# Optimization experiments

Measured on AMD Instinct MI355X. Metric: run time of the kernel, lower is better.

Reference implementation:

```python
import jax, jax.numpy as jnp
import numpy as np
from jax import lax

B, T, S = 32, 64, 400
H, E, EMB, V = 512, 1024, 256, 32000


def setup_inputs() -> dict:
    key = jax.random.key(0)
    ks = jax.random.split(key, 16)
    w = lambda k, shape: jax.random.normal(k, shape, dtype=jnp.float32) * 0.05
    return {
        "target": jax.random.randint(ks[0], (B, T), 0, V),
        "h0": jax.random.normal(ks[1], (B, H), dtype=jnp.float32),
        "c0": jax.random.normal(ks[2], (B, H), dtype=jnp.float32),
        "enc_outs": jax.random.normal(ks[3], (S, B, E), dtype=jnp.float32),
        "attn_mask": jnp.ones((B, S), dtype=jnp.int32),
        "emb": w(ks[4], (V, EMB)),
        "W_ih": w(ks[5], (4 * H, EMB)),
        "b_ih": w(ks[6], (4 * H,)),
        "W_hh": w(ks[7], (4 * H, H)),
        "b_hh": w(ks[8], (4 * H,)),
        "W_attn": w(ks[9], (H, E)),
        "b_attn": w(ks[10], (H,)),
        "W_concat": w(ks[11], (H, E + H)),
        "b_concat": w(ks[12], (H,)),
        "W_out": w(ks[13], (V, H)),
        "b_out": w(ks[14], (V,)),
    }


def reference(target, h0, c0, enc_outs, attn_mask, emb, W_ih, b_ih, W_hh, b_hh,
              W_attn, b_attn, W_concat, b_concat, W_out, b_out):
    # Precompute attention keys projection once: [S, B, H]
    keys_proj = jnp.einsum("sbe,he->sbh", enc_outs, W_attn) + b_attn
    masked = attn_mask == 0  # [B, S]
    x_seq = emb[target].transpose(1, 0, 2)  # [T, B, EMB]

    def step(carry, x_t):
        h, c = carry
        # LSTMCell (torch gate order: i, f, g, o)
        gates = x_t @ W_ih.T + b_ih + h @ W_hh.T + b_hh  # [B, 4H]
        i, f, g, o = jnp.split(gates, 4, axis=1)
        c = jax.nn.sigmoid(f) * c + jax.nn.sigmoid(i) * jnp.tanh(g)
        h = jax.nn.sigmoid(o) * jnp.tanh(c)
        # additive-style attention: sum over hidden of query*key_proj
        scores = jnp.einsum("bh,sbh->bs", h, keys_proj)  # [B, S]
        scores = jnp.where(masked, jnp.float32(-1e18), scores)
        a = jax.nn.softmax(scores, axis=1)
        ctx = jnp.einsum("bs,sbe->be", a, enc_outs)  # [B, E]
        cat = jnp.tanh(jnp.concatenate([ctx, h], axis=1) @ W_concat.T + b_concat)
        logit = jax.nn.log_softmax(cat @ W_out.T + b_out, axis=-1)  # [B, V]
        return (h, c), logit

    (_, _), logits = lax.scan(step, (h0, c0), x_seq)  # [T, B, V]
    return logits.transpose(1, 0, 2)  # [B, T, V]
```

## Files before the change

kernel.cpp:

```cpp
#include <hip/hip_runtime.h>
#include <hip/hip_bf16.h>
#include <hip/hip_fp16.h>

#define B_ 32
#define T_ 64
#define S_ 400
#define SPAD_ 512
#define H_ 512
#define E_ 1024
#define EMB_ 256
#define V_ 32000
#define NCB_ 500

#define KEYS_BLOCKS 200
#define CVT_BLOCKS 48
#define MEGA_BLOCKS (8 + KEYS_BLOCKS + CVT_BLOCKS)
#define MEGA_LDS (65536 + 33280 + 4096 + 32)

typedef _Float16 f16;
typedef _Float16 half8 __attribute__((ext_vector_type(8)));
typedef float f32x4 __attribute__((ext_vector_type(4)));
typedef float f32x16 __attribute__((ext_vector_type(16)));
typedef unsigned uint4v __attribute__((ext_vector_type(4)));

__device__ __forceinline__ void gl_lds16(const void* g, void* l) {
  __builtin_amdgcn_global_load_lds(
      (const __attribute__((address_space(1))) void*)g,
      (__attribute__((address_space(3))) void*)l, 16, 0, 0);
}

__device__ __forceinline__ float sigmoidf_(float x) { return 1.f / (1.f + expf(-x)); }

__device__ __forceinline__ uint4v load_b128_sys(const void* p) {
  uint4v r;
  asm volatile("global_load_dwordx4 %0, %1, off sc0 sc1" : "=v"(r) : "v"(p) : "memory");
  return r;
}
__device__ __forceinline__ void store_b128_sys(void* p, uint4v v) {
  asm volatile("global_store_dwordx4 %0, %1, off sc0 sc1" :: "v"(p), "v"(v) : "memory");
}

__global__ __launch_bounds__(256) void prep_kernel(const float* __restrict__ b_ih,
                                                   const float* __restrict__ b_hh,
                                                   float* __restrict__ biasperm,
                                                   const float* __restrict__ Whh,
                                                   f16* __restrict__ Wperm,
                                                   const float* __restrict__ Wih,
                                                   f16* __restrict__ Wihp,
                                                   const float* __restrict__ h0,
                                                   f16* __restrict__ hbuf,
                                                   const float* __restrict__ Wattn,
                                                   f16* __restrict__ Wattn_f,
                                                   const int* __restrict__ target,
                                                   const float* __restrict__ emb,
                                                   f16* __restrict__ xin) {
  int idx = blockIdx.x * 256 + threadIdx.x;
  if (idx < 4 * H_) {
    int j = idx >> 2, gg = idx & 3;
    biasperm[idx] = b_ih[gg * H_ + j] + b_hh[gg * H_ + j];
  }
  if (idx < B_ * H_) hbuf[idx] = (f16)h0[idx];
  if (idx < T_ * B_ * H_ / 8) {
    uint4v p = {0xFFFFFFFFu, 0xFFFFFFFFu, 0xFFFFFFFFu, 0xFFFFFFFFu};
    reinterpret_cast<uint4v*>(reinterpret_cast<char*>(hbuf) + (size_t)B_ * H_ * 2)[idx] = p;
  }
  {
    int j = idx >> 9, k = idx & 511;
#pragma unroll
    for (int gg = 0; gg < 4; ++gg)
      Wperm[((size_t)(j * 4 + gg)) * H_ + k] = (f16)Whh[((size_t)(gg * H_ + j)) * H_ + k];
  }
  if (idx < H_ * EMB_) {
    int j = idx >> 8, k = idx & 255;
#pragma unroll
    for (int gg = 0; gg < 4; ++gg)
      Wihp[((size_t)(j * 4 + gg)) * EMB_ + k] = (f16)Wih[((size_t)(gg * H_ + j)) * EMB_ + k];
  }
  {
    float2 v = reinterpret_cast<const float2*>(Wattn)[idx];
    union { f16 h[2]; unsigned u; } o;
    o.h[0] = (f16)v.x; o.h[1] = (f16)v.y;
    reinterpret_cast<unsigned*>(Wattn_f)[idx] = o.u;
  }
  {
    int rr = idx >> 7, cc = (idx & 127) * 2;
    int t = rr >> 5, bb = rr & 31;
    int tok = target[bb * T_ + t];
    float2 ev = *reinterpret_cast<const float2*>(emb + (size_t)tok * EMB_ + cc);
    union { f16 h[2]; unsigned u; } o2;
    o2.h[0] = (f16)ev.x; o2.h[1] = (f16)ev.y;
    *reinterpret_cast<unsigned*>(xin + (size_t)rr * EMB_ + cc) = o2.u;
  }
}

template <int OUTK, bool DO_TANH>
__global__ __launch_bounds__(256) void gemm_bt_kernel(const f16* __restrict__ A,
                                                      const f16* __restrict__ W,
                                                      const float* __restrict__ bias,
                                                      void* __restrict__ outp,
                                                      int M, int N, int K) {
  __shared__ __align__(16) char As[128 * 64];
  __shared__ __align__(16) char Bs[128 * 64];
  const int tid = threadIdx.x;
  const int lane = tid & 63, wave = tid >> 6;
  const int wr = (wave >> 1) * 64, wc = (wave & 1) * 64;
  const int fr = lane & 15, fq = lane >> 4;
  const int row0 = blockIdx.x * 128, col0 = blockIdx.y * 128;

  f32x4 acc[4][4];
#pragma unroll
  for (int i = 0; i < 4; ++i)
#pragma unroll
    for (int j = 0; j < 4; ++j) acc[i][j] = {0.f, 0.f, 0.f, 0.f};

  for (int k0 = 0; k0 < K; k0 += 32) {
    __syncthreads();
#pragma unroll
    for (int i = 0; i < 2; ++i) {
      int o = tid * 16 + i * 4096;
      int r = o >> 6, kk = (o & 63) >> 1;
      gl_lds16(A + (size_t)(row0 + r) * K + (k0 + kk), As + o);
      gl_lds16(W + (size_t)(col0 + r) * K + (k0 + kk), Bs + o);
    }
    __syncthreads();
    half8 af[4], bfr[4];
#pragma unroll
    for (int mi = 0; mi < 4; ++mi)
      af[mi] = *reinterpret_cast<const half8*>(As + (wr + mi * 16 + fr) * 64 + fq * 16);
#pragma unroll
    for (int ni = 0; ni < 4; ++ni)
      bfr[ni] = *reinterpret_cast<const half8*>(Bs + (wc + ni * 16 + fr) * 64 + fq * 16);
#pragma unroll
    for (int mi = 0; mi < 4; ++mi)
#pragma unroll
      for (int ni = 0; ni < 4; ++ni)
        acc[mi][ni] = __builtin_amdgcn_mfma_f32_16x16x32_f16(af[mi], bfr[ni], acc[mi][ni], 0, 0, 0);
  }

#pragma unroll
  for (int mi = 0; mi < 4; ++mi)
#pragma unroll
    for (int ni = 0; ni < 4; ++ni)
#pragma unroll
      for (int r = 0; r < 4; ++r) {
        int row = row0 + wr + mi * 16 + fq * 4 + r;
        int col = col0 + wc + ni * 16 + fr;
        float v = acc[mi][ni][r] + bias[col];
        if (DO_TANH) v = tanhf(v);
        if (OUTK == 0) {
          ((float*)outp)[(size_t)row * N + col] = v;
        } else if (OUTK == 1) {
          ((f16*)outp)[(size_t)row * N + col] = (f16)v;
        } else {
          int orow = (row & 31) * T_ + (row >> 5);
          ((float*)outp)[(size_t)orow * N + col] = v;
        }
      }
}

__global__ __launch_bounds__(512, 1) void mega_kernel(
    const float* __restrict__ xpart, const f16* __restrict__ Wperm,
    const float* __restrict__ c0, f16* __restrict__ hbuf,
    const float* __restrict__ enc, const f16* __restrict__ Wattn_f,
    const float* __restrict__ b_attn, f16* __restrict__ keys,
    const float* __restrict__ wc_src, f16* __restrict__ wc_dst,
    const float* __restrict__ wo_src, f16* __restrict__ wo_dst) {
  extern __shared__ char lds[];
  const int blk = blockIdx.x, tid = threadIdx.x;
  const int lane = tid & 63, wave = tid >> 6;

  if (blk < 8) {
    char* Abuf = lds;
    float* gates = (float*)(lds + 65536);
    unsigned* hstage = (unsigned*)(lds + 65536 + 33280);
    int* flags = (int*)(lds + 65536 + 33280 + 4096);
    const int g = blk;
    const int ln31 = lane & 31, lh = lane >> 5;

    if (tid < 8) flags[tid] = 0;

    half8 wf[32];
    {
      const f16* wrow = Wperm + ((size_t)(g * 256 + wave * 32 + ln31)) * H_ + lh * 8;
#pragma unroll
      for (int kc = 0; kc < 32; ++kc)
        wf[kc] = *reinterpret_cast<const half8*>(wrow + kc * 16);
    }

    const int b = tid >> 4, qd = tid & 15;
    float cst[4];
#pragma unroll
    for (int jj = 0; jj < 4; ++jj)
      cst[jj] = c0[b * H_ + g * 64 + qd * 4 + jj];

    __syncthreads();

    for (int t = 0; t < T_; ++t) {
      const float* xr = xpart + ((size_t)(t * B_ + b)) * (4 * H_) + g * 256 + qd * 16;
      float4 xv[4];
#pragma unroll
      for (int i = 0; i < 4; ++i) xv[i] = *reinterpret_cast<const float4*>(xr + i * 4);

      {
        int p = (t == 0) ? wave : (wave + (wave >= g ? 1 : 0));
        bool duty = (t == 0) ? true : (wave < 7);
        if (duty) {
          const char* sb = (const char*)hbuf + (size_t)t * 32768 + ln31 * 1024 + p * 128 + lh * 16;
          while (true) {
            uint4v v0 = load_b128_sys(sb);
            uint4v v1 = load_b128_sys(sb + 32);
            uint4v v2 = load_b128_sys(sb + 64);
            uint4v v3 = load_b128_sys(sb + 96);
            asm volatile("s_waitcnt vmcnt(0)" ::: "memory");
            __builtin_amdgcn_sched_barrier(0);
            unsigned bad = 0;
#pragma unroll
            for (int d = 0; d < 4; ++d)
              bad |= (unsigned)(v0[d] == 0xFFFFFFFFu) | (unsigned)(v1[d] == 0xFFFFFFFFu) |
                     (unsigned)(v2[d] == 0xFFFFFFFFu) | (unsigned)(v3[d] == 0xFFFFFFFFu);
            if (__all(bad == 0)) {
              char* ab = Abuf + (size_t)(t & 1) * 32768 + lane * 16;
              *(uint4v*)(ab + (size_t)(4 * p + 0) * 1024) = v0;
              *(uint4v*)(ab + (size_t)(4 * p + 1) * 1024) = v1;
              *(uint4v*)(ab + (size_t)(4 * p + 2) * 1024) = v2;
              *(uint4v*)(ab + (size_t)(4 * p + 3) * 1024) = v3;
              asm volatile("s_waitcnt lgkmcnt(0)" ::: "memory");
              __builtin_amdgcn_sched_barrier(0);
              if (lane == 0)
                __hip_atomic_fetch_add(&flags[p], 1, __ATOMIC_RELAXED,
                                       __HIP_MEMORY_SCOPE_WORKGROUP);
              break;
            }
          }
        }
      }

      f32x16 acc;
#pragma unroll
      for (int r = 0; r < 16; ++r) acc[r] = 0.f;
      const char* abR = Abuf + (size_t)(t & 1) * 32768 + lane * 16;
      const char* hsR = (const char*)hstage + lane * 16;
      const int thr = t + 1;
#pragma unroll
      for (int ps = 0; ps < 8; ++ps) {
        if (ps == g && t > 0) {
#pragma unroll
          for (int c = 0; c < 4; ++c) {
            half8 a = *(const half8*)(hsR + c * 1024);
            acc = __builtin_amdgcn_mfma_f32_32x32x16_f16(a, wf[4 * ps + c], acc, 0, 0, 0);
          }
        } else {
          while (__hip_atomic_load(&flags[ps], __ATOMIC_ACQUIRE,
                                   __HIP_MEMORY_SCOPE_WORKGROUP) < thr) {}
#pragma unroll
          for (int c = 0; c < 4; ++c) {
            half8 a = *(const half8*)(abR + (size_t)(4 * ps + c) * 1024);
            acc = __builtin_amdgcn_mfma_f32_32x32x16_f16(a, wf[4 * ps + c], acc, 0, 0, 0);
          }
        }
      }
#pragma unroll
      for (int r = 0; r < 16; ++r) {
        int row = (r & 3) + 8 * (r >> 2) + 4 * lh;
        gates[row * 260 + wave * 32 + ln31] = acc[r];
      }
      __syncthreads();

      const float* gr = &gates[b * 260 + qd * 16];
      float hv[4];
#pragma unroll
      for (int jj = 0; jj < 4; ++jj) {
        float gi = gr[jj * 4 + 0] + xv[jj].x;
        float gf = gr[jj * 4 + 1] + xv[jj].y;
        float gg = gr[jj * 4 + 2] + xv[jj].z;
        float go = gr[jj * 4 + 3] + xv[jj].w;
        cst[jj] = sigmoidf_(gf) * cst[jj] + sigmoidf_(gi) * tanhf(gg);
        hv[jj] = sigmoidf_(go) * tanhf(cst[jj]);
      }
      union { f16 h[2]; unsigned u; } pk0, pk1;
      pk0.h[0] = (f16)hv[0]; pk0.h[1] = (f16)hv[1];
      pk1.h[0] = (f16)hv[2]; pk1.h[1] = (f16)hv[3];
      {
        int cp0 = 2 * qd, cp1 = 2 * qd + 1;
        hstage[((cp0 >> 3) * 64 + ((cp0 >> 2) & 1) * 32 + b) * 4 + (cp0 & 3)] = pk0.u;
        hstage[((cp1 >> 3) * 64 + ((cp1 >> 2) & 1) * 32 + b) * 4 + (cp1 & 3)] = pk1.u;
      }
      __syncthreads();

      if (tid < 256) {
        int kcl = tid >> 6, l2 = tid & 63;
        uint4v v = *(const uint4v*)((const char*)hstage + (kcl * 64 + l2) * 16);
        store_b128_sys((char*)hbuf + (size_t)(t + 1) * 32768 + (l2 & 31) * 1024 +
                           g * 128 + kcl * 32 + (l2 >> 5) * 16,
                       v);
      }
    }
  } else if (blk < 8 + KEYS_BLOCKS) {
    char* As = lds;
    char* Bs = lds + 16384;
    const int kid = blk - 8;
    const int row0 = (kid % 50) * 256, col0 = (kid / 50) * 128;
    const int wr = (wave >> 1) * 64, wc = (wave & 1) * 64;
    const int fr = lane & 15, fq = lane >> 4;

    f32x4 acc[4][4];
#pragma unroll
    for (int i = 0; i < 4; ++i)
#pragma unroll
      for (int j = 0; j < 4; ++j) acc[i][j] = {0.f, 0.f, 0.f, 0.f};

    for (int k0 = 0; k0 < E_; k0 += 32) {
      __syncthreads();
      float4 av[4];
#pragma unroll
      for (int i = 0; i < 4; ++i) {
        int idx = tid + i * 512;
        int r = idx >> 3, ck = (idx & 7) * 4;
        av[i] = *reinterpret_cast<const float4*>(enc + (size_t)(row0 + r) * E_ + k0 + ck);
      }
      {
        int o = tid * 16;
        int r = o >> 6, kk = (o & 63) >> 1;
        gl_lds16(Wattn_f + (size_t)(col0 + r) * E_ + (k0 + kk), Bs + o);
      }
#pragma unroll
      for (int i = 0; i < 4; ++i) {
        int idx = tid + i * 512;
        int r = idx >> 3, ck = (idx & 7) * 4;
        union { f16 h[4]; unsigned long long u; } p;
        p.h[0] = (f16)av[i].x; p.h[1] = (f16)av[i].y;
        p.h[2] = (f16)av[i].z; p.h[3] = (f16)av[i].w;
        *reinterpret_cast<unsigned long long*>(As + r * 64 + ck * 2) = p.u;
      }
      __syncthreads();
      half8 af[4], bf[4];
#pragma unroll
      for (int mi = 0; mi < 4; ++mi)
        af[mi] = *reinterpret_cast<const half8*>(As + (wr + mi * 16 + fr) * 64 + fq * 16);
#pragma unroll
      for (int ni = 0; ni < 4; ++ni)
        bf[ni] = *reinterpret_cast<const half8*>(Bs + (wc + ni * 16 + fr) * 64 + fq * 16);
#pragma unroll
      for (int mi = 0; mi < 4; ++mi)
#pragma unroll
        for (int ni = 0; ni < 4; ++ni)
          acc[mi][ni] = __builtin_amdgcn_mfma_f32_16x16x32_f16(af[mi], bf[ni], acc[mi][ni], 0, 0, 0);
    }
#pragma unroll
    for (int mi = 0; mi < 4; ++mi)
#pragma unroll
      for (int ni = 0; ni < 4; ++ni)
#pragma unroll
        for (int r = 0; r < 4; ++r) {
          int row = row0 + wr + mi * 16 + fq * 4 + r;
          int col = col0 + wc + ni * 16 + fr;
          keys[(size_t)row * H_ + col] = (f16)(acc[mi][ni][r] + b_attn[col]);
        }
  } else {
    const int N2WC = H_ * (E_ + H_) / 2, N2WO = V_ * H_ / 2;
    const int total = N2WC + N2WO;
    const int stride = CVT_BLOCKS * 512;
    for (int i = (blk - 8 - KEYS_BLOCKS) * 512 + tid; i < total; i += stride) {
      const float* s; f16* d; int j;
      if (i < N2WC) { s = wc_src; d = wc_dst; j = i; }
      else { s = wo_src; d = wo_dst; j = i - N2WC; }
      float2 v = reinterpret_cast<const float2*>(s)[j];
      union { f16 h[2]; unsigned u; } o;
      o.h[0] = (f16)v.x; o.h[1] = (f16)v.y;
      reinterpret_cast<unsigned*>(d)[j] = o.u;
    }
  }
}

__global__ __launch_bounds__(256) void scores_mfma_kernel(const f16* __restrict__ keys,
                                                          const f16* __restrict__ hseq,
                                                          float* __restrict__ attnw) {
  const int b = blockIdx.y;
  const int lane = threadIdx.x & 63, wave = threadIdx.x >> 6;
  const int ln31 = lane & 31, lh = lane >> 5;
  const int stile = blockIdx.x * 128 + wave * 32;
  const f16* ar  = keys + ((size_t)(stile + ln31) * B_ + b) * H_ + lh * 8;
  const f16* br0 = hseq + ((size_t)ln31 * B_ + b) * H_ + lh * 8;
  const f16* br1 = hseq + ((size_t)(ln31 + 32) * B_ + b) * H_ + lh * 8;
  f32x16 ac0, ac1;
#pragma unroll
  for (int r = 0; r < 16; ++r) { ac0[r] = 0.f; ac1[r] = 0.f; }
#pragma unroll
  for (int kc = 0; kc < 32; ++kc) {
    half8 a  = *reinterpret_cast<const half8*>(ar + kc * 16);
    half8 h0 = *reinterpret_cast<const half8*>(br0 + kc * 16);
    half8 h1 = *reinterpret_cast<const half8*>(br1 + kc * 16);
    ac0 = __builtin_amdgcn_mfma_f32_32x32x16_f16(a, h0, ac0, 0, 0, 0);
    ac1 = __builtin_amdgcn_mfma_f32_32x32x16_f16(a, h1, ac1, 0, 0, 0);
  }
#pragma unroll
  for (int r = 0; r < 16; ++r) {
    int s = stile + (r & 3) + 8 * (r >> 2) + 4 * lh;
    if (s < S_) {
      attnw[((size_t)b * S_ + s) * T_ + ln31]      = ac0[r];
      attnw[((size_t)b * S_ + s) * T_ + 32 + ln31] = ac1[r];
    }
  }
}

__global__ __launch_bounds__(64) void softmax_kernel(float* __restrict__ attnw,
                                                     const int* __restrict__ mask) {
  int b = blockIdx.x, t = blockIdx.y, l = threadIdx.x;
  float vals[7];
  float m = -3.4e38f;
#pragma unroll
  for (int i = 0; i < 7; ++i) {
    int s = l + i * 64;
    float v = -3.4e38f;
    if (s < S_) {
      v = attnw[((size_t)b * S_ + s) * T_ + t];
      if (mask[b * S_ + s] == 0) v = -1e18f;
    }
    vals[i] = v;
    m = fmaxf(m, v);
  }
#pragma unroll
  for (int o = 32; o > 0; o >>= 1) m = fmaxf(m, __shfl_xor(m, o));
  float sum = 0.f;
#pragma unroll
  for (int i = 0; i < 7; ++i) {
    int s = l + i * 64;
    if (s < S_) { float e = expf(vals[i] - m); vals[i] = e; sum += e; }
  }
#pragma unroll
  for (int o = 32; o > 0; o >>= 1) sum += __shfl_xor(sum, o);
  float inv = 1.f / sum;
#pragma unroll
  for (int i = 0; i < 7; ++i) {
    int s = l + i * 64;
    if (s < S_) attnw[((size_t)b * S_ + s) * T_ + t] = vals[i] * inv;
  }
}

__global__ __launch_bounds__(256) void ctx_cat_kernel(const float* __restrict__ attnw,
                                                      const float* __restrict__ enc,
                                                      const f16* __restrict__ hseq,
                                                      f16* __restrict__ catin) {
  int b = blockIdx.x, y = blockIdx.y;
  if (y == 16) {
    for (int i = threadIdx.x; i < 64 * 64; i += 256) {
      int t = i >> 6, c = i & 63;
      uint4v v = *(const uint4v*)((const char*)hseq + ((size_t)t * B_ + b) * 1024 + c * 16);
      *(uint4v*)((char*)catin + ((size_t)t * B_ + b) * 3072 + 2048 + c * 16) = v;
    }
    return;
  }
  int e0 = y * 64;
  int el = threadIdx.x & 63, tq = threadIdx.x >> 6;
  __shared__ float a_lds[100 * 64];
  float acc[16];
#pragma unroll
  for (int i = 0; i < 16; ++i) acc[i] = 0.f;
  for (int scn = 0; scn < 4; ++scn) {
    __syncthreads();
    for (int i = threadIdx.x; i < 6400; i += 256)
      a_lds[i] = attnw[((size_t)b * S_ + scn * 100) * T_ + i];
    __syncthreads();
    for (int sl = 0; sl < 100; ++sl) {
      int s = scn * 100 + sl;
      float v = enc[((size_t)s * B_ + b) * E_ + e0 + el];
#pragma unroll
      for (int i = 0; i < 16; ++i) acc[i] += a_lds[sl * 64 + tq * 16 + i] * v;
    }
  }
#pragma unroll
  for (int i = 0; i < 16; ++i) {
    int t = tq * 16 + i;
    catin[((size_t)t * B_ + b) * (E_ + H_) + e0 + el] = (f16)acc[i];
  }
}

__global__ __launch_bounds__(512) void gemm_out256_kernel(const f16* __restrict__ A,
                                                          const f16* __restrict__ W,
                                                          const float* __restrict__ bias,
                                                          f16* __restrict__ lbuf,
                                                          float* __restrict__ pm,
                                                          float* __restrict__ ps) {
  __shared__ __align__(16) char As[256 * 64];
  __shared__ __align__(16) char Bs[128 * 64];
  const int tid = threadIdx.x;
  const int lane = tid & 63, wave = tid >> 6;
  const int wr = (wave >> 1) * 64, wc = (wave & 1) * 64;
  const int fr = lane & 15, fq = lane >> 4;
  const int row0 = blockIdx.x * 256, col0 = blockIdx.y * 128;

  f32x4 acc[4][4];
#pragma unroll
  for (int i = 0; i < 4; ++i)
#pragma unroll
    for (int j = 0; j < 4; ++j) acc[i][j] = {0.f, 0.f, 0.f, 0.f};

  for (int k0 = 0; k0 < H_; k0 += 32) {
    __syncthreads();
    {
      int o = tid * 16;
      int r = o >> 6, kk = (o & 63) >> 1;
      gl_lds16(A + (size_t)(row0 + r) * H_ + (k0 + kk), As + o);
      gl_lds16(W + (size_t)(col0 + r) * H_ + (k0 + kk), Bs + o);
      o += 8192; r = o >> 6; kk = (o & 63) >> 1;
      gl_lds16(A + (size_t)(row0 + r) * H_ + (k0 + kk), As + o);
    }
    __syncthreads();
    half8 af[4], bfr[4];
#pragma unroll
    for (int mi = 0; mi < 4; ++mi)
      af[mi] = *reinterpret_cast<const half8*>(As + (wr + mi * 16 + fr) * 64 + fq * 16);
#pragma unroll
    for (int ni = 0; ni < 4; ++ni)
      bfr[ni] = *reinterpret_cast<const half8*>(Bs + (wc + ni * 16 + fr) * 64 + fq * 16);
#pragma unroll
    for (int mi = 0; mi < 4; ++mi)
#pragma unroll
      for (int ni = 0; ni < 4; ++ni)
        acc[mi][ni] = __builtin_amdgcn_mfma_f32_16x16x32_f16(af[mi], bfr[ni], acc[mi][ni], 0, 0, 0);
  }

#pragma unroll
  for (int mi = 0; mi < 4; ++mi)
#pragma unroll
    for (int r = 0; r < 4; ++r) {
      int row = row0 + wr + mi * 16 + fq * 4 + r;
      float v0 = acc[mi][0][r] + bias[col0 + wc + fr];
      float v1 = acc[mi][1][r] + bias[col0 + wc + 16 + fr];
      float v2 = acc[mi][2][r] + bias[col0 + wc + 32 + fr];
      float v3 = acc[mi][3][r] + bias[col0 + wc + 48 + fr];
      f16* lp = lbuf + (size_t)row * V_ + col0 + wc + fr;
      lp[0] = (f16)v0; lp[16] = (f16)v1; lp[32] = (f16)v2; lp[48] = (f16)v3;
      float mx = fmaxf(fmaxf(v0, v1), fmaxf(v2, v3));
#pragma unroll
      for (int d2 = 1; d2 <= 8; d2 <<= 1) mx = fmaxf(mx, __shfl_xor(mx, d2));
      float sm = expf(v0 - mx) + expf(v1 - mx) + expf(v2 - mx) + expf(v3 - mx);
#pragma unroll
      for (int d2 = 1; d2 <= 8; d2 <<= 1) sm += __shfl_xor(sm, d2);
      if (fr == 0) {
        int cb = (col0 + wc) >> 6;
        pm[(size_t)row * NCB_ + cb] = mx;
        ps[(size_t)row * NCB_ + cb] = sm;
      }
    }
}

__global__ __launch_bounds__(256) void final_out_kernel(const f16* __restrict__ lbuf,
                                                        const float* __restrict__ pm,
                                                        const float* __restrict__ ps,
                                                        float* __restrict__ out) {
  int j = blockIdx.x;
  int b = j >> 6, t = j & 63;
  int r = t * B_ + b;
  int tid = threadIdx.x;
  __shared__ float red[4];
  __shared__ float lsh;

  float mv0 = -3.4e38f, sv0 = 0.f, mv1 = -3.4e38f, sv1 = 0.f;
  if (tid < NCB_) { mv0 = pm[(size_t)r * NCB_ + tid]; sv0 = ps[(size_t)r * NCB_ + tid]; }
  int i2 = tid + 256;
  if (i2 < NCB_) { mv1 = pm[(size_t)r * NCB_ + i2]; sv1 = ps[(size_t)r * NCB_ + i2]; }
  float m = fmaxf(mv0, mv1);
#pragma unroll
  for (int o = 32; o > 0; o >>= 1) m = fmaxf(m, __shfl_xor(m, o));
  if ((tid & 63) == 0) red[tid >> 6] = m;
  __syncthreads();
  float mm = fmaxf(fmaxf(red[0], red[1]), fmaxf(red[2], red[3]));
  float s = sv0 * expf(mv0 - mm) + sv1 * expf(mv1 - mm);
#pragma unroll
  for (int o = 32; o > 0; o >>= 1) s += __shfl_xor(s, o);
  __syncthreads();
  if ((tid & 63) == 0) red[tid >> 6] = s;
  __syncthreads();
  if (tid == 0) lsh = mm + logf(red[0] + red[1] + red[2] + red[3]);
  __syncthreads();
  float l = lsh;

  const half8* src = reinterpret_cast<const half8*>(lbuf + (size_t)r * V_);
  float4* dst = reinterpret_cast<float4*>(out + (size_t)j * V_);
  for (int c = tid; c < V_ / 8; c += 256) {
    half8 h = src[c];
    float4 o1, o2;
    o1.x = (float)h[0] - l; o1.y = (float)h[1] - l;
    o1.z = (float)h[2] - l; o1.w = (float)h[3] - l;
    o2.x = (float)h[4] - l; o2.y = (float)h[5] - l;
    o2.z = (float)h[6] - l; o2.w = (float)h[7] - l;
    dst[c * 2] = o1; dst[c * 2 + 1] = o2;
  }
}

__global__ __launch_bounds__(512, 1) void logsm_kernel(float* __restrict__ out) {
  int r = blockIdx.x;
  size_t base = (size_t)r * V_;
  int tid = threadIdx.x;
  float4* op = reinterpret_cast<float4*>(out + base);
  float4 v[16];
  float m = -3.4e38f;
#pragma unroll
  for (int k = 0; k < 16; ++k) {
    int c = tid + (k << 9);
    if (c < 8000) {
      v[k] = op[c];
      m = fmaxf(m, fmaxf(fmaxf(v[k].x, v[k].y), fmaxf(v[k].z, v[k].w)));
    }
  }
  __shared__ float red[8];
#pragma unroll
  for (int o = 32; o > 0; o >>= 1) m = fmaxf(m, __shfl_xor(m, o));
  if ((tid & 63) == 0) red[tid >> 6] = m;
  __syncthreads();
  float mm = red[0];
#pragma unroll
  for (int i = 1; i < 8; ++i) mm = fmaxf(mm, red[i]);
  float s = 0.f;
#pragma unroll
  for (int k = 0; k < 16; ++k) {
    int c = tid + (k << 9);
    if (c < 8000)
      s += expf(v[k].x - mm) + expf(v[k].y - mm) + expf(v[k].z - mm) + expf(v[k].w - mm);
  }
#pragma unroll
  for (int o = 32; o > 0; o >>= 1) s += __shfl_xor(s, o);
  __syncthreads();
  if ((tid & 63) == 0) red[tid >> 6] = s;
  __syncthreads();
  s = 0.f;
#pragma unroll
  for (int i = 0; i < 8; ++i) s += red[i];
  float lse = mm + logf(s);
#pragma unroll
  for (int k = 0; k < 16; ++k) {
    int c = tid + (k << 9);
    if (c < 8000) {
      float4 o4;
      o4.x = v[k].x - lse; o4.y = v[k].y - lse;
      o4.z = v[k].z - lse; o4.w = v[k].w - lse;
      op[c] = o4;
    }
  }
}

extern "C" void kernel_launch(void* const* d_in, const int* in_sizes, int n_in,
                              void* d_out, int out_size, void* d_ws, size_t ws_size,
                              hipStream_t stream) {
  const int*   target = (const int*)d_in[0];
  const float* h0     = (const float*)d_in[1];
  const float* c0     = (const float*)d_in[2];
  const float* enc    = (const float*)d_in[3];
  const int*   mask   = (const int*)d_in[4];
  const float* emb    = (const float*)d_in[5];
  const float* W_ih   = (const float*)d_in[6];
  const float* b_ih   = (const float*)d_in[7];
  const float* W_hh   = (const float*)d_in[8];
  const float* b_hh   = (const float*)d_in[9];
  const float* W_attn = (const float*)d_in[10];
  const float* b_attn = (const float*)d_in[11];
  const float* W_cat  = (const float*)d_in[12];
  const float* b_cat  = (const float*)d_in[13];
  const float* W_out  = (const float*)d_in[14];
  const float* b_out  = (const float*)d_in[15];

  char* ws = (char*)d_ws;
  size_t off = 0;
  auto alloc = [&](size_t bytes) {
    void* p = ws + off;
    off = (off + bytes + 255) & ~(size_t)255;
    return p;
  };
  f16*   keys_f   = (f16*)alloc((size_t)SPAD_ * B_ * H_ * 2);
  f16*   Wattn_f  = (f16*)alloc((size_t)H_ * E_ * 2);
  f16*   Wcat_f   = (f16*)alloc((size_t)H_ * (E_ + H_) * 2);
  f16*   Wout_f   = (f16*)alloc((size_t)V_ * H_ * 2);
  f16*   Wperm    = (f16*)alloc((size_t)4 * H_ * H_ * 2);
  f16*   Wihp     = (f16*)alloc((size_t)4 * H_ * EMB_ * 2);
  float* biasperm = (float*)alloc((size_t)4 * H_ * 4);
  f16*   xin_f    = (f16*)alloc((size_t)T_ * B_ * EMB_ * 2);
  float* xpart    = (float*)alloc((size_t)T_ * B_ * 4 * H_ * 4);
  f16*   catin_f  = (f16*)alloc((size_t)T_ * B_ * (E_ + H_) * 2);
  float* attnw    = (float*)alloc((size_t)B_ * S_ * T_ * 4);
  f16*   catbuf_f = (f16*)alloc((size_t)T_ * B_ * H_ * 2);
  f16*   hbuf     = (f16*)alloc((size_t)(T_ + 1) * B_ * H_ * 2);

  size_t extra = ((size_t)T_ * B_ * V_ * 2 + 255 + (size_t)T_ * B_ * NCB_ * 4 * 2 + 512);
  bool pathA = (off + extra) <= ws_size;
  f16* lbuf = nullptr; float* pm = nullptr; float* psb = nullptr;
  if (pathA) {
    lbuf = (f16*)alloc((size_t)T_ * B_ * V_ * 2);
    pm   = (float*)alloc((size_t)T_ * B_ * NCB_ * 4);
    psb  = (float*)alloc((size_t)T_ * B_ * NCB_ * 4);
  }
  (void)in_sizes; (void)n_in; (void)out_size;

  f16* hseq_f = hbuf + (size_t)B_ * H_;

  prep_kernel<<<(H_ * H_) / 256, 256, 0, stream>>>(b_ih, b_hh, biasperm, W_hh, Wperm,
                                                   W_ih, Wihp, h0, hbuf, W_attn, Wattn_f,
                                                   target, emb, xin_f);
  gemm_bt_kernel<0, false><<<dim3((T_ * B_) / 128, (4 * H_) / 128), 256, 0, stream>>>(
      xin_f, Wihp, biasperm, xpart, T_ * B_, 4 * H_, EMB_);

  mega_kernel<<<MEGA_BLOCKS, 512, MEGA_LDS, stream>>>(
      xpart, Wperm, c0, hbuf, enc, Wattn_f, b_attn, keys_f,
      W_cat, Wcat_f, W_out, Wout_f);

  scores_mfma_kernel<<<dim3(SPAD_ / 128, B_), 256, 0, stream>>>(keys_f, hseq_f, attnw);
  softmax_kernel<<<dim3(B_, T_), 64, 0, stream>>>(attnw, mask);
  ctx_cat_kernel<<<dim3(B_, 17), 256, 0, stream>>>(attnw, enc, hseq_f, catin_f);

  gemm_bt_kernel<1, true><<<dim3((T_ * B_) / 128, H_ / 128), 256, 0, stream>>>(
      catin_f, Wcat_f, b_cat, catbuf_f, T_ * B_, H_, E_ + H_);

  if (pathA) {
    gemm_out256_kernel<<<dim3((T_ * B_) / 256, V_ / 128), 512, 0, stream>>>(
        catbuf_f, Wout_f, b_out, lbuf, pm, psb);
    final_out_kernel<<<T_ * B_, 256, 0, stream>>>(lbuf, pm, psb, (float*)d_out);
  } else {
    gemm_bt_kernel<2, false><<<dim3((T_ * B_) / 128, V_ / 128), 256, 0, stream>>>(
        catbuf_f, Wout_f, b_out, (float*)d_out, T_ * B_, V_, H_);
    logsm_kernel<<<B_ * T_, 512, 0, stream>>>((float*)d_out);
  }
}
```

Measured before the change: 718.6 us.

## Fuse prep and input-projection GEMM, batch softmax rows, swizzle output GEMM blocks

```diff
diff --git a/kernel.cpp b/kernel.cpp
--- a/kernel.cpp
+++ b/kernel.cpp
@@ -40,56 +40,111 @@
   asm volatile("global_store_dwordx4 %0, %1, off sc0 sc1" :: "v"(p), "v"(v) : "memory");
 }
 
-__global__ __launch_bounds__(256) void prep_kernel(const float* __restrict__ b_ih,
-                                                   const float* __restrict__ b_hh,
-                                                   float* __restrict__ biasperm,
-                                                   const float* __restrict__ Whh,
-                                                   f16* __restrict__ Wperm,
-                                                   const float* __restrict__ Wih,
-                                                   f16* __restrict__ Wihp,
-                                                   const float* __restrict__ h0,
-                                                   f16* __restrict__ hbuf,
-                                                   const float* __restrict__ Wattn,
-                                                   f16* __restrict__ Wattn_f,
-                                                   const int* __restrict__ target,
-                                                   const float* __restrict__ emb,
-                                                   f16* __restrict__ xin) {
-  int idx = blockIdx.x * 256 + threadIdx.x;
-  if (idx < 4 * H_) {
-    int j = idx >> 2, gg = idx & 3;
-    biasperm[idx] = b_ih[gg * H_ + j] + b_hh[gg * H_ + j];
-  }
-  if (idx < B_ * H_) hbuf[idx] = (f16)h0[idx];
-  if (idx < T_ * B_ * H_ / 8) {
-    uint4v p = {0xFFFFFFFFu, 0xFFFFFFFFu, 0xFFFFFFFFu, 0xFFFFFFFFu};
-    reinterpret_cast<uint4v*>(reinterpret_cast<char*>(hbuf) + (size_t)B_ * H_ * 2)[idx] = p;
-  }
-  {
-    int j = idx >> 9, k = idx & 511;
-#pragma unroll
-    for (int gg = 0; gg < 4; ++gg)
-      Wperm[((size_t)(j * 4 + gg)) * H_ + k] = (f16)Whh[((size_t)(gg * H_ + j)) * H_ + k];
-  }
-  if (idx < H_ * EMB_) {
-    int j = idx >> 8, k = idx & 255;
-#pragma unroll
-    for (int gg = 0; gg < 4; ++gg)
-      Wihp[((size_t)(j * 4 + gg)) * EMB_ + k] = (f16)Wih[((size_t)(gg * H_ + j)) * EMB_ + k];
-  }
-  {
-    float2 v = reinterpret_cast<const float2*>(Wattn)[idx];
-    union { f16 h[2]; unsigned u; } o;
-    o.h[0] = (f16)v.x; o.h[1] = (f16)v.y;
-    reinterpret_cast<unsigned*>(Wattn_f)[idx] = o.u;
-  }
-  {
-    int rr = idx >> 7, cc = (idx & 127) * 2;
-    int t = rr >> 5, bb = rr & 31;
-    int tok = target[bb * T_ + t];
-    float2 ev = *reinterpret_cast<const float2*>(emb + (size_t)tok * EMB_ + cc);
-    union { f16 h[2]; unsigned u; } o2;
-    o2.h[0] = (f16)ev.x; o2.h[1] = (f16)ev.y;
-    *reinterpret_cast<unsigned*>(xin + (size_t)rr * EMB_ + cc) = o2.u;
+__device__ __forceinline__ unsigned long long pack8f16(float4 a, float4 b) {
+  union { f16 h[4]; unsigned long long u; } p;
+  p.h[0] = (f16)a.x; p.h[1] = (f16)a.y; p.h[2] = (f16)a.z; p.h[3] = (f16)a.w;
+  unsigned long long lo = p.u;
+  p.h[0] = (f16)b.x; p.h[1] = (f16)b.y; p.h[2] = (f16)b.z; p.h[3] = (f16)b.w;
+  return lo | 0ull;
+}
+
+__global__ __launch_bounds__(256) void prep_xpart_kernel(
+    const int* __restrict__ target, const float* __restrict__ emb,
+    const float* __restrict__ Wih, const float* __restrict__ b_ih,
+    const float* __restrict__ b_hh, float* __restrict__ xpart,
+    const float* __restrict__ Whh, f16* __restrict__ Wperm,
+    const float* __restrict__ h0, f16* __restrict__ hbuf,
+    const float* __restrict__ Wattn, f16* __restrict__ Wattn_f) {
+  const int blk = blockIdx.x, tid = threadIdx.x;
+  if (blk < 256) {
+    __shared__ __align__(16) char As[128 * 64];
+    __shared__ __align__(16) char Bs[128 * 64];
+    const int lane = tid & 63, wave = tid >> 6;
+    const int wr = (wave >> 1) * 64, wc = (wave & 1) * 64;
+    const int fr = lane & 15, fq = lane >> 4;
+    const int row0 = (blk & 15) * 128, col0 = (blk >> 4) * 128;
+
+    f32x4 acc[4][4];
+#pragma unroll
+    for (int i = 0; i < 4; ++i)
+#pragma unroll
+      for (int j = 0; j < 4; ++j) acc[i][j] = {0.f, 0.f, 0.f, 0.f};
+
+    for (int k0 = 0; k0 < EMB_; k0 += 32) {
+      __syncthreads();
+#pragma unroll
+      for (int it = 0; it < 2; ++it) {
+        int idx = tid + it * 256;
+        int r = idx >> 2, cq = idx & 3;
+        int t = (row0 + r) >> 5, b = (row0 + r) & 31;
+        int tok = target[b * T_ + t];
+        const float* ap = emb + (size_t)tok * EMB_ + k0 + cq * 8;
+        float4 a0 = *reinterpret_cast<const float4*>(ap);
+        float4 a1 = *reinterpret_cast<const float4*>(ap + 4);
+        union { f16 h[8]; unsigned long long u[2]; } pa;
+#pragma unroll
+        for (int q = 0; q < 4; ++q) { pa.h[q] = (f16)((const float*)&a0)[q]; pa.h[4 + q] = (f16)((const float*)&a1)[q]; }
+        *reinterpret_cast<unsigned long long*>(As + r * 64 + cq * 16) = pa.u[0];
+        *reinterpret_cast<unsigned long long*>(As + r * 64 + cq * 16 + 8) = pa.u[1];
+        int c = col0 + r;
+        int orig = (c & 3) * 512 + (c >> 2);
+        const float* bp = Wih + (size_t)orig * EMB_ + k0 + cq * 8;
+        float4 b0 = *reinterpret_cast<const float4*>(bp);
+        float4 b1 = *reinterpret_cast<const float4*>(bp + 4);
+        union { f16 h[8]; unsigned long long u[2]; } pb;
+#pragma unroll
+        for (int q = 0; q < 4; ++q) { pb.h[q] = (f16)((const float*)&b0)[q]; pb.h[4 + q] = (f16)((const float*)&b1)[q]; }
+        *reinterpret_cast<unsigned long long*>(Bs + r * 64 + cq * 16) = pb.u[0];
+        *reinterpret_cast<unsigned long long*>(Bs + r * 64 + cq * 16 + 8) = pb.u[1];
+      }
+      __syncthreads();
+      half8 af[4], bfr[4];
+#pragma unroll
+      for (int mi = 0; mi < 4; ++mi)
+        af[mi] = *reinterpret_cast<const half8*>(As + (wr + mi * 16 + fr) * 64 + fq * 16);
+#pragma unroll
+      for (int ni = 0; ni < 4; ++ni)
+        bfr[ni] = *reinterpret_cast<const half8*>(Bs + (wc + ni * 16 + fr) * 64 + fq * 16);
+#pragma unroll
+      for (int mi = 0; mi < 4; ++mi)
+#pragma unroll
+        for (int ni = 0; ni < 4; ++ni)
+          acc[mi][ni] = __builtin_amdgcn_mfma_f32_16x16x32_f16(af[mi], bfr[ni], acc[mi][ni], 0, 0, 0);
+    }
+#pragma unroll
+    for (int mi = 0; mi < 4; ++mi)
+#pragma unroll
+      for (int ni = 0; ni < 4; ++ni) {
+        int col = col0 + wc + ni * 16 + fr;
+        int orig = (col & 3) * 512 + (col >> 2);
+        float bias = b_ih[orig] + b_hh[orig];
+#pragma unroll
+        for (int r = 0; r < 4; ++r) {
+          int row = row0 + wr + mi * 16 + fq * 4 + r;
+          xpart[(size_t)row * 2048 + col] = acc[mi][ni][r] + bias;
+        }
+      }
+  } else {
+    const int base = (blk - 256) * 256 + tid;
+    const int stride = 64 * 256;
+    for (int idx = base; idx < H_ * H_; idx += stride) {
+      int j = idx >> 9, k = idx & 511;
+#pragma unroll
+      for (int gg = 0; gg < 4; ++gg)
+        Wperm[((size_t)(j * 4 + gg)) * H_ + k] = (f16)Whh[((size_t)(gg * H_ + j)) * H_ + k];
+    }
+    for (int idx = base; idx < H_ * E_ / 2; idx += stride) {
+      float2 v = reinterpret_cast<const float2*>(Wattn)[idx];
+      union { f16 h[2]; unsigned u; } o;
+      o.h[0] = (f16)v.x; o.h[1] = (f16)v.y;
+      reinterpret_cast<unsigned*>(Wattn_f)[idx] = o.u;
+    }
+    for (int idx = base; idx < T_ * B_ * H_ / 8; idx += stride) {
+      uint4v p = {0xFFFFFFFFu, 0xFFFFFFFFu, 0xFFFFFFFFu, 0xFFFFFFFFu};
+      reinterpret_cast<uint4v*>(reinterpret_cast<char*>(hbuf) + (size_t)B_ * H_ * 2)[idx] = p;
+    }
+    for (int idx = base; idx < B_ * H_; idx += stride)
+      hbuf[idx] = (f16)h0[idx];
   }
 }
 
@@ -403,9 +458,10 @@
   }
 }
 
-__global__ __launch_bounds__(64) void softmax_kernel(float* __restrict__ attnw,
-                                                     const int* __restrict__ mask) {
-  int b = blockIdx.x, t = blockIdx.y, l = threadIdx.x;
+__global__ __launch_bounds__(256) void softmax_kernel(float* __restrict__ attnw,
+                                                      const int* __restrict__ mask) {
+  int b = blockIdx.x, t = blockIdx.y * 4 + (threadIdx.x >> 6);
+  int l = threadIdx.x & 63;
   float vals[7];
   float m = -3.4e38f;
 #pragma unroll
@@ -487,7 +543,9 @@
   const int lane = tid & 63, wave = tid >> 6;
   const int wr = (wave >> 1) * 64, wc = (wave & 1) * 64;
   const int fr = lane & 15, fq = lane >> 4;
-  const int row0 = blockIdx.x * 256, col0 = blockIdx.y * 128;
+  const int k = blockIdx.x + blockIdx.y * 8;
+  const int p = (k % 8) * 250 + k / 8;
+  const int row0 = (p % 8) * 256, col0 = (p / 8) * 128;
 
   f32x4 acc[4][4];
 #pragma unroll
@@ -672,9 +730,6 @@
   f16*   Wcat_f   = (f16*)alloc((size_t)H_ * (E_ + H_) * 2);
   f16*   Wout_f   = (f16*)alloc((size_t)V_ * H_ * 2);
   f16*   Wperm    = (f16*)alloc((size_t)4 * H_ * H_ * 2);
-  f16*   Wihp     = (f16*)alloc((size_t)4 * H_ * EMB_ * 2);
-  float* biasperm = (float*)alloc((size_t)4 * H_ * 4);
-  f16*   xin_f    = (f16*)alloc((size_t)T_ * B_ * EMB_ * 2);
   float* xpart    = (float*)alloc((size_t)T_ * B_ * 4 * H_ * 4);
   f16*   catin_f  = (f16*)alloc((size_t)T_ * B_ * (E_ + H_) * 2);
   float* attnw    = (float*)alloc((size_t)B_ * S_ * T_ * 4);
@@ -693,25 +748,22 @@
 
   f16* hseq_f = hbuf + (size_t)B_ * H_;
 
-  prep_kernel<<<(H_ * H_) / 256, 256, 0, stream>>>(b_ih, b_hh, biasperm, W_hh, Wperm,
-                                                   W_ih, Wihp, h0, hbuf, W_attn, Wattn_f,
-                                                   target, emb, xin_f);
-  gemm_bt_kernel<0, false><<<dim3((T_ * B_) / 128, (4 * H_) / 128), 256, 0, stream>>>(
-      xin_f, Wihp, biasperm, xpart, T_ * B_, 4 * H_, EMB_);
+  prep_xpart_kernel<<<320, 256, 0, stream>>>(target, emb, W_ih, b_ih, b_hh, xpart,
+                                             W_hh, Wperm, h0, hbuf, W_attn, Wattn_f);
 
   mega_kernel<<<MEGA_BLOCKS, 512, MEGA_LDS, stream>>>(
       xpart, Wperm, c0, hbuf, enc, Wattn_f, b_attn, keys_f,
       W_cat, Wcat_f, W_out, Wout_f);
 
   scores_mfma_kernel<<<dim3(SPAD_ / 128, B_), 256, 0, stream>>>(keys_f, hseq_f, attnw);
-  softmax_kernel<<<dim3(B_, T_), 64, 0, stream>>>(attnw, mask);
+  softmax_kernel<<<dim3(B_, 16), 256, 0, stream>>>(attnw, mask);
   ctx_cat_kernel<<<dim3(B_, 17), 256, 0, stream>>>(attnw, enc, hseq_f, catin_f);
 
   gemm_bt_kernel<1, true><<<dim3((T_ * B_) / 128, H_ / 128), 256, 0, stream>>>(
       catin_f, Wcat_f, b_cat, catbuf_f, T_ * B_, H_, E_ + H_);
 
   if (pathA) {
-    gemm_out256_kernel<<<dim3((T_ * B_) / 256, V_ / 128), 512, 0, stream>>>(
+    gemm_out256_kernel<<<dim3(8, 250), 512, 0, stream>>>(
         catbuf_f, Wout_f, b_out, lbuf, pm, psb);
     final_out_kernel<<<T_ * B_, 256, 0, stream>>>(lbuf, pm, psb, (float*)d_out);
   } else {
```

Result: no change. 724.6 us (+0.8%).
